# Optimization experiments

Hardware: AMD Instinct MI355X
Metric: run time of the kernel (lower is better)

The kernel has to match this reference:

```python
import jax, jax.numpy as jnp
import numpy as np

NUM_BINS = 256
EPS = 1e-08


def setup_inputs() -> dict:
    key = jax.random.key(0)
    k1, k2 = jax.random.split(key)
    B, C, H, W = 16, 3, 512, 512
    pred = jax.random.uniform(k1, (B, C, H, W), dtype=jnp.float32)
    target = jax.random.uniform(k2, (B, C, H, W), dtype=jnp.float32)
    return {"pred": pred, "target": target}


def _compute_histogram(x):
    """Per-(batch, channel) 256-bin histogram of values in [0, 1].

    Faithful to torch.histc(bins=N, min=0, max=1): bin width 1/N,
    value v -> bin floor(v*N), with v == 1.0 landing in the last bin
    (handled by the clip). Values outside [0,1] are ignored.
    Implemented as a single fused scatter-add over all B*C histograms.
    """
    B, C, H, W = x.shape
    in_range = (x >= 0.0) & (x <= 1.0)
    bins = jnp.clip(jnp.floor(x * NUM_BINS).astype(jnp.int32), 0, NUM_BINS - 1)
    # flat index into [B*C, NUM_BINS] histogram array
    bc = jnp.arange(B * C, dtype=jnp.int32)[:, None]  # [B*C, 1]
    flat_idx = (bc * NUM_BINS + bins.reshape(B * C, H * W)).reshape(-1)
    weights = in_range.reshape(-1).astype(x.dtype)
    hist = jnp.zeros(B * C * NUM_BINS, dtype=x.dtype).at[flat_idx].add(weights)
    return hist.reshape(B, C, NUM_BINS)


def reference(pred, target):
    pred_hist = _compute_histogram(pred)
    target_hist = _compute_histogram(target)
    pred_hist = pred_hist / (pred_hist.sum(axis=2, keepdims=True) + EPS)
    target_hist = target_hist / (target_hist.sum(axis=2, keepdims=True) + EPS)
    return jnp.mean((pred_hist - target_hist) ** 2)
```

## Files before the change

### kernel.cpp

```cpp
#include <hip/hip_runtime.h>

#define NUM_BINS 256
#define PLANES 48
#define PLANE_ELEMS (512 * 512)
#define BPP 16
#define THREADS 256
#define F4_PER_BLOCK (PLANE_ELEMS / 4 / BPP)
#define F4_PER_THREAD (F4_PER_BLOCK / THREADS)
#define NSUB 16
#define HSTRIDE 257
#define BATCH 4

__global__ __launch_bounds__(THREADS) void hist_kernel(const float* __restrict__ pred,
                                                       const float* __restrict__ target,
                                                       unsigned* __restrict__ part,
                                                       unsigned* __restrict__ counter) {
    __shared__ alignas(16) unsigned lh[NSUB * HSTRIDE];
    const int t = threadIdx.x;
    const int lane = t & 63;
    const int gid = blockIdx.x;

    if (gid == 0 && t == 0) *counter = 0u;

    uint4* l4 = reinterpret_cast<uint4*>(lh);
    for (int i = t; i < (NSUB * HSTRIDE) / 4; i += THREADS) l4[i] = make_uint4(0, 0, 0, 0);
    __syncthreads();

    const int which = gid / (PLANES * BPP);
    const int rem   = gid - which * (PLANES * BPP);
    const int plane = rem / BPP;
    const int cblk  = rem - plane * BPP;

    const float* src = which ? target : pred;
    const float4* p = reinterpret_cast<const float4*>(src + (size_t)plane * PLANE_ELEMS)
                      + (size_t)cblk * F4_PER_BLOCK;

    unsigned* sub = lh + (size_t)(lane & (NSUB - 1)) * HSTRIDE;

    float4 cur[BATCH], nxt[BATCH];
#pragma unroll
    for (int j = 0; j < BATCH; ++j) cur[j] = p[j * THREADS + t];

    for (int c = 0; c < F4_PER_THREAD / BATCH; ++c) {
        if (c + 1 < F4_PER_THREAD / BATCH) {
#pragma unroll
            for (int j = 0; j < BATCH; ++j)
                nxt[j] = p[(c + 1) * BATCH * THREADS + j * THREADS + t];
        }
#pragma unroll
        for (int j = 0; j < BATCH; ++j) {
            float e[4] = {cur[j].x, cur[j].y, cur[j].z, cur[j].w};
#pragma unroll
            for (int k = 0; k < 4; ++k) {
                int b = (int)(e[k] * 256.0f);
                b = b > 255 ? 255 : b;
                atomicAdd(&sub[b], 1u);
            }
        }
#pragma unroll
        for (int j = 0; j < BATCH; ++j) cur[j] = nxt[j];
    }
    __syncthreads();

    unsigned c = 0;
#pragma unroll
    for (int h = 0; h < NSUB; ++h) c += lh[h * HSTRIDE + t];
    part[(size_t)gid * NUM_BINS + t] = c;
}

__global__ __launch_bounds__(THREADS) void reduce_kernel(const unsigned* __restrict__ part,
                                                         double* __restrict__ plane_loss,
                                                         unsigned* __restrict__ counter,
                                                         float* __restrict__ out) {
    __shared__ unsigned wa[4], wb[4];
    __shared__ double sd[THREADS];
    __shared__ unsigned sh_old;
    const int t = threadIdx.x;
    const int p = blockIdx.x;

    const unsigned* bp = part + (size_t)p * BPP * NUM_BINS;
    const unsigned* bt = part + (size_t)(PLANES + p) * BPP * NUM_BINS;
    unsigned hp = 0, ht = 0;
#pragma unroll
    for (int j = 0; j < BPP; ++j) {
        hp += bp[j * NUM_BINS + t];
        ht += bt[j * NUM_BINS + t];
    }

    unsigned a = hp, b = ht;
    for (int off = 32; off; off >>= 1) {
        a += __shfl_down(a, off, 64);
        b += __shfl_down(b, off, 64);
    }
    if ((t & 63) == 0) { wa[t >> 6] = a; wb[t >> 6] = b; }
    __syncthreads();
    const unsigned Sp = wa[0] + wa[1] + wa[2] + wa[3];
    const unsigned St = wb[0] + wb[1] + wb[2] + wb[3];

    const double ip = 1.0 / ((double)Sp + 1e-8);
    const double it = 1.0 / ((double)St + 1e-8);
    const double d = (double)hp * ip - (double)ht * it;
    sd[t] = d * d;
    __syncthreads();
    for (int off = THREADS / 2; off; off >>= 1) {
        if (t < off) sd[t] += sd[t + off];
        __syncthreads();
    }

    if (t == 0) {
        plane_loss[p] = sd[0];
        __threadfence();
        sh_old = atomicAdd(counter, 1u);
    }
    __syncthreads();

    if (sh_old == PLANES - 1) {
        __threadfence();
        if (t < 64) {
            double v = (t < PLANES) ? plane_loss[t] : 0.0;
            for (int off = 32; off; off >>= 1) v += __shfl_down(v, off, 64);
            if (t == 0) out[0] = (float)(v / (double)(PLANES * NUM_BINS));
        }
    }
}

extern "C" void kernel_launch(void* const* d_in, const int* in_sizes, int n_in,
                              void* d_out, int out_size, void* d_ws, size_t ws_size,
                              hipStream_t stream) {
    const float* pred   = (const float*)d_in[0];
    const float* target = (const float*)d_in[1];
    float* out = (float*)d_out;
    unsigned* part = (unsigned*)d_ws;
    double* plane_loss = reinterpret_cast<double*>(
        (char*)d_ws + (size_t)2 * PLANES * BPP * NUM_BINS * sizeof(unsigned));
    unsigned* counter = reinterpret_cast<unsigned*>(plane_loss + PLANES);

    hist_kernel<<<2 * PLANES * BPP, THREADS, 0, stream>>>(pred, target, part, counter);
    reduce_kernel<<<PLANES, THREADS, 0, stream>>>(part, plane_loss, counter, out);
}
```

Measured before the change: 26.53 us.

## Split blocks between LDS-atomic and wave-ballot histogram paths

```diff
diff --git a/kernel.cpp b/kernel.cpp
--- a/kernel.cpp
+++ b/kernel.cpp
@@ -7,7 +7,7 @@
 #define THREADS 256
 #define F4_PER_BLOCK (PLANE_ELEMS / 4 / BPP)
 #define F4_PER_THREAD (F4_PER_BLOCK / THREADS)
-#define NSUB 16
+#define NSUB 8
 #define HSTRIDE 257
 #define BATCH 4
 
@@ -18,13 +18,10 @@
     __shared__ alignas(16) unsigned lh[NSUB * HSTRIDE];
     const int t = threadIdx.x;
     const int lane = t & 63;
+    const int w = t >> 6;
     const int gid = blockIdx.x;
 
     if (gid == 0 && t == 0) *counter = 0u;
-
-    uint4* l4 = reinterpret_cast<uint4*>(lh);
-    for (int i = t; i < (NSUB * HSTRIDE) / 4; i += THREADS) l4[i] = make_uint4(0, 0, 0, 0);
-    __syncthreads();
 
     const int which = gid / (PLANES * BPP);
     const int rem   = gid - which * (PLANES * BPP);
@@ -35,37 +32,108 @@
     const float4* p = reinterpret_cast<const float4*>(src + (size_t)plane * PLANE_ELEMS)
                       + (size_t)cblk * F4_PER_BLOCK;
 
-    unsigned* sub = lh + (size_t)(lane & (NSUB - 1)) * HSTRIDE;
-
-    float4 cur[BATCH], nxt[BATCH];
-#pragma unroll
-    for (int j = 0; j < BATCH; ++j) cur[j] = p[j * THREADS + t];
-
-    for (int c = 0; c < F4_PER_THREAD / BATCH; ++c) {
-        if (c + 1 < F4_PER_THREAD / BATCH) {
-#pragma unroll
-            for (int j = 0; j < BATCH; ++j)
-                nxt[j] = p[(c + 1) * BATCH * THREADS + j * THREADS + t];
+    const bool ballot_blk = (((gid >> 3) & 15) < 9);
+
+    if (!ballot_blk) {
+        uint4* l4 = reinterpret_cast<uint4*>(lh);
+        for (int i = t; i < (NSUB * HSTRIDE + 3) / 4; i += THREADS) l4[i] = make_uint4(0, 0, 0, 0);
+        __syncthreads();
+
+        unsigned* sub = lh + (size_t)(lane & (NSUB - 1)) * HSTRIDE;
+
+        float4 cur[BATCH], nxt[BATCH];
+#pragma unroll
+        for (int j = 0; j < BATCH; ++j) cur[j] = p[j * THREADS + t];
+
+        for (int c = 0; c < F4_PER_THREAD / BATCH; ++c) {
+            if (c + 1 < F4_PER_THREAD / BATCH) {
+#pragma unroll
+                for (int j = 0; j < BATCH; ++j)
+                    nxt[j] = p[(c + 1) * BATCH * THREADS + j * THREADS + t];
+            }
+#pragma unroll
+            for (int j = 0; j < BATCH; ++j) {
+                float e[4] = {cur[j].x, cur[j].y, cur[j].z, cur[j].w};
+#pragma unroll
+                for (int k = 0; k < 4; ++k) {
+                    int b = (int)(e[k] * 256.0f);
+                    b = b > 255 ? 255 : b;
+                    atomicAdd(&sub[b], 1u);
+                }
+            }
+#pragma unroll
+            for (int j = 0; j < BATCH; ++j) cur[j] = nxt[j];
         }
-#pragma unroll
-        for (int j = 0; j < BATCH; ++j) {
-            float e[4] = {cur[j].x, cur[j].y, cur[j].z, cur[j].w};
-#pragma unroll
-            for (int k = 0; k < 4; ++k) {
-                int b = (int)(e[k] * 256.0f);
-                b = b > 255 ? 255 : b;
-                atomicAdd(&sub[b], 1u);
-            }
+        __syncthreads();
+
+        unsigned c = 0;
+#pragma unroll
+        for (int h = 0; h < NSUB; ++h) c += lh[h * HSTRIDE + t];
+        part[(size_t)gid * NUM_BINS + t] = c;
+    } else {
+        const unsigned m0 = ((lane >> 0) & 1) ? 0u : ~0u;
+        const unsigned m1 = ((lane >> 1) & 1) ? 0u : ~0u;
+        const unsigned m2 = ((lane >> 2) & 1) ? 0u : ~0u;
+        const unsigned m3 = ((lane >> 3) & 1) ? 0u : ~0u;
+        const unsigned m4 = ((lane >> 4) & 1) ? 0u : ~0u;
+        const unsigned m5 = ((lane >> 5) & 1) ? 0u : ~0u;
+        unsigned c0 = 0, c1 = 0, c2 = 0, c3 = 0;
+
+#define ROUND(xx)                                                                 \
+    do {                                                                          \
+        float x = (xx);                                                           \
+        int b = (int)(x * 256.0f);                                                \
+        b = b > 255 ? 255 : b;                                                    \
+        unsigned long long B1 = __ballot(b & 2);                                  \
+        unsigned long long B2 = __ballot(b & 4);                                  \
+        unsigned long long B3 = __ballot(b & 8);                                  \
+        unsigned long long B4 = __ballot(b & 16);                                 \
+        unsigned long long B5 = __ballot(b & 32);                                 \
+        unsigned long long B6 = __ballot(b & 64);                                 \
+        unsigned long long B0 = __ballot(b & 1);                                  \
+        unsigned long long B7 = __ballot(b & 128);                                \
+        unsigned long long Te0 = ~B0 & ~B7, Te1 = B0 & ~B7;                       \
+        unsigned long long Te2 = ~B0 &  B7, Te3 = B0 &  B7;                       \
+        unsigned lo = ((unsigned)B1 ^ m0) & ((unsigned)B2 ^ m1) &                 \
+                      ((unsigned)B3 ^ m2) & ((unsigned)B4 ^ m3) &                 \
+                      ((unsigned)B5 ^ m4) & ((unsigned)B6 ^ m5);                  \
+        unsigned hi = ((unsigned)(B1 >> 32) ^ m0) & ((unsigned)(B2 >> 32) ^ m1) & \
+                      ((unsigned)(B3 >> 32) ^ m2) & ((unsigned)(B4 >> 32) ^ m3) & \
+                      ((unsigned)(B5 >> 32) ^ m4) & ((unsigned)(B6 >> 32) ^ m5);  \
+        c0 += __popc(lo & (unsigned)Te0) + __popc(hi & (unsigned)(Te0 >> 32));    \
+        c1 += __popc(lo & (unsigned)Te1) + __popc(hi & (unsigned)(Te1 >> 32));    \
+        c2 += __popc(lo & (unsigned)Te2) + __popc(hi & (unsigned)(Te2 >> 32));    \
+        c3 += __popc(lo & (unsigned)Te3) + __popc(hi & (unsigned)(Te3 >> 32));    \
+    } while (0)
+
+        float4 cur[BATCH], nxt[BATCH];
+#pragma unroll
+        for (int j = 0; j < BATCH; ++j) cur[j] = p[j * THREADS + t];
+
+        for (int c = 0; c < F4_PER_THREAD / BATCH; ++c) {
+            if (c + 1 < F4_PER_THREAD / BATCH) {
+#pragma unroll
+                for (int j = 0; j < BATCH; ++j)
+                    nxt[j] = p[(c + 1) * BATCH * THREADS + j * THREADS + t];
+            }
+#pragma unroll
+            for (int j = 0; j < BATCH; ++j) {
+                ROUND(cur[j].x); ROUND(cur[j].y); ROUND(cur[j].z); ROUND(cur[j].w);
+            }
+#pragma unroll
+            for (int j = 0; j < BATCH; ++j) cur[j] = nxt[j];
         }
-#pragma unroll
-        for (int j = 0; j < BATCH; ++j) cur[j] = nxt[j];
-    }
-    __syncthreads();
-
-    unsigned c = 0;
-#pragma unroll
-    for (int h = 0; h < NSUB; ++h) c += lh[h * HSTRIDE + t];
-    part[(size_t)gid * NUM_BINS + t] = c;
+#undef ROUND
+
+        unsigned long long* st64 = reinterpret_cast<unsigned long long*>(lh + w * NUM_BINS);
+        st64[lane]      = (unsigned long long)c0 | ((unsigned long long)c1 << 32);
+        st64[64 + lane] = (unsigned long long)c2 | ((unsigned long long)c3 << 32);
+        __syncthreads();
+
+        unsigned c = lh[0 * NUM_BINS + t] + lh[1 * NUM_BINS + t]
+                   + lh[2 * NUM_BINS + t] + lh[3 * NUM_BINS + t];
+        part[(size_t)gid * NUM_BINS + t] = c;
+    }
 }
 
 __global__ __launch_bounds__(THREADS) void reduce_kernel(const unsigned* __restrict__ part,
```

Result: slower. 48.84 us (+84.1%).
